# Kernel tuning notes

Hardware: AMD Instinct MI355X
Metric: run time of the kernel (lower is better)

The kernel has to match this reference:

```python
import jax, jax.numpy as jnp
import numpy as np

NUM_HEADS = 12
EMB = 768
D_KEY = 64
D_VALUE = 64
MASKED = True


def setup_inputs() -> dict:
    key = jax.random.key(0)
    k1, k2, k3, k4 = jax.random.split(key, 4)
    x = jax.random.normal(k1, (1, 4096, EMB), dtype=jnp.float32)
    q_proj = jax.random.normal(k2, (NUM_HEADS, EMB, D_KEY), dtype=jnp.float32)
    k_proj = jax.random.normal(k3, (NUM_HEADS, EMB, D_KEY), dtype=jnp.float32)
    v_proj = jax.random.normal(k4, (NUM_HEADS, EMB, D_VALUE), dtype=jnp.float32)
    return {"x": x, "q_proj": q_proj, "k_proj": k_proj, "v_proj": v_proj}


def reference(x, q_proj, k_proj, v_proj):
    # x: [B, S, E]; projections: [H, E, dk/dv]
    q = jnp.einsum("bse,hek->bhsk", x, q_proj)  # [B,H,S,dk]
    k = jnp.einsum("bse,hek->bhsk", x, k_proj)  # [B,H,S,dk]
    v = jnp.einsum("bse,hev->bhsv", x, v_proj)  # [B,H,S,dv]
    scale = jnp.sqrt(jnp.asarray(D_KEY, dtype=x.dtype))
    scores = jnp.einsum("bhsk,bhtk->bhst", q, k) / scale  # [B,H,S,S]
    if MASKED:
        S = x.shape[1]
        # causal mask: disallow attending to future positions (strict upper triangle)
        mask = jnp.triu(jnp.ones((S, S), dtype=bool), k=1)
        scores = jnp.where(mask, -jnp.inf, scores)
    attn = jax.nn.softmax(scores, axis=-1)
    out = jnp.einsum("bhst,bhtv->bhsv", attn, v)  # [B,H,S,dv]
    return out
```

## Files before the change

### kernel.cpp

```cpp
#include <hip/hip_runtime.h>
#include <hip/hip_bf16.h>

#define NH 12
#define SEQ 4096
#define E 768
#define DK 64

typedef float f32x4 __attribute__((ext_vector_type(4)));
typedef float f32x16 __attribute__((ext_vector_type(16)));
typedef __bf16 bf16x8 __attribute__((ext_vector_type(8)));
typedef __bf16 bf16x4 __attribute__((ext_vector_type(4)));
typedef unsigned u32x2 __attribute__((ext_vector_type(2)));
typedef unsigned u32x4 __attribute__((ext_vector_type(4)));

#define MFMA16(a, b, c) __builtin_amdgcn_mfma_f32_16x16x32_bf16((a), (b), (c), 0, 0, 0)
#define MFMA32(a, b, c) __builtin_amdgcn_mfma_f32_32x32x16_bf16((a), (b), (c), 0, 0, 0)

#define SCL 0.18033688011112042f
#define DEFER 10.8f

#define PART_SZ 4352
#define TPH 144

__device__ __forceinline__ void gload16(const void* g, void* l) {
    __builtin_amdgcn_global_load_lds(
        (const __attribute__((address_space(1))) void*)g,
        (__attribute__((address_space(3))) void*)l, 16, 0, 0);
}

__device__ __forceinline__ void block_sync() {
    __builtin_amdgcn_sched_barrier(0);
    __builtin_amdgcn_s_barrier();
    __builtin_amdgcn_sched_barrier(0);
}

__device__ __forceinline__ unsigned cvtpk(float lo, float hi) {
    unsigned r;
    asm("v_cvt_pk_bf16_f32 %0, %1, %2" : "=v"(r) : "v"(lo), "v"(hi));
    return r;
}
__device__ __forceinline__ u32x2 plswap(unsigned a, unsigned b) {
    return __builtin_amdgcn_permlane32_swap(a, b, false, false);
}
__device__ __forceinline__ float xhalf_max(float v) {
    u32x2 r = plswap(__float_as_uint(v), __float_as_uint(v));
    return fmaxf(__uint_as_float(r.x), __uint_as_float(r.y));
}
__device__ __forceinline__ float xhalf_add(float v) {
    u32x2 r = plswap(__float_as_uint(v), __float_as_uint(v));
    return __uint_as_float(r.x) + __uint_as_float(r.y);
}

__global__ __launch_bounds__(256) void xsplit_kernel(const float* __restrict__ x,
                                                     __bf16* __restrict__ xh,
                                                     __bf16* __restrict__ xl) {
    int i = blockIdx.x * blockDim.x + threadIdx.x;
    float4 v = ((const float4*)x)[i];
    bf16x4 h, l;
    float vv[4] = {v.x, v.y, v.z, v.w};
#pragma unroll
    for (int j = 0; j < 4; ++j) {
        __bf16 hh = (__bf16)vv[j];
        h[j] = hh;
        l[j] = (__bf16)(vv[j] - (float)hh);
    }
    ((bf16x4*)xh)[i] = h;
    ((bf16x4*)xl)[i] = l;
}

__global__ void wsplit_kernel(const float* __restrict__ qp,
                              const float* __restrict__ kp,
                              const float* __restrict__ vp,
                              __bf16* __restrict__ wtq_h, __bf16* __restrict__ wtq_l,
                              __bf16* __restrict__ wtk_h, __bf16* __restrict__ wtk_l,
                              __bf16* __restrict__ wtv_h) {
    int idx = blockIdx.x * blockDim.x + threadIdx.x;
    if (idx >= NH * E * DK) return;
    int h = idx / (E * DK);
    int rem = idx - h * E * DK;
    int k = rem / DK;
    int n = rem - k * DK;
    int o = h * DK * E + n * E + k;
    float q = qp[idx];
    __bf16 qh = (__bf16)q;
    wtq_h[o] = qh;
    wtq_l[o] = (__bf16)(q - (float)qh);
    float kk = kp[idx] * SCL;
    __bf16 kh = (__bf16)kk;
    wtk_h[o] = kh;
    wtk_l[o] = (__bf16)(kk - (float)kh);
    wtv_h[o] = (__bf16)vp[idx];
}

__global__ __launch_bounds__(256, 2) void proj_kernel(
    const __bf16* __restrict__ xh, const __bf16* __restrict__ xl,
    const __bf16* __restrict__ wq_h_g, const __bf16* __restrict__ wq_l_g,
    const __bf16* __restrict__ wk_h_g, const __bf16* __restrict__ wk_l_g,
    const __bf16* __restrict__ wv_g,
    __bf16* __restrict__ qh_o, __bf16* __restrict__ ql_o,
    __bf16* __restrict__ kh_o, __bf16* __restrict__ kl_o,
    __bf16* __restrict__ vt_o) {
    __shared__ char wlds[2][20480];

    const int wg = (blockIdx.x & 7) * 96 + (blockIdx.x >> 3);
    const int head = wg >> 6;
    const int rb = wg & 63;
    const int wave = threadIdx.x >> 6;
    const int lane = threadIdx.x & 63;
    const int lrow = lane & 15;
    const int lk8 = (lane >> 4) * 8;
    const int g4 = (lane >> 4) * 4;
    const int rowbase = rb * 64 + wave * 16;

    const char* bases[5] = {
        (const char*)(wq_h_g + head * DK * E), (const char*)(wq_l_g + head * DK * E),
        (const char*)(wk_h_g + head * DK * E), (const char*)(wk_l_g + head * DK * E),
        (const char*)(wv_g + head * DK * E)};
    const int srow = lane >> 2;
    const int scol = (lane & 3) * 16;

    auto STAGE = [&](int buf, int ks) {
#pragma unroll
        for (int r = 0; r < 5; ++r) {
            int q = wave * 5 + r;
            const char* src = bases[q >> 2] + (size_t)((q & 3) * 16 + srow) * (E * 2) + ks * 64 + scol;
            gload16(src, wlds[buf] + q * 1024 + lane * 16);
        }
    };

    f32x4 accq[4], acck[4], accv[4];
#pragma unroll
    for (int f = 0; f < 4; ++f) {
        accq[f] = (f32x4){0.f, 0.f, 0.f, 0.f};
        acck[f] = (f32x4){0.f, 0.f, 0.f, 0.f};
        accv[f] = (f32x4){0.f, 0.f, 0.f, 0.f};
    }

    bf16x8 ah, al, ahn, aln;
    auto LOADA = [&](int ks, bf16x8& h, bf16x8& l) {
        size_t xo = (size_t)(rowbase + lrow) * E + ks * 32 + lk8;
        h = *(const bf16x8*)(xh + xo);
        l = *(const bf16x8*)(xl + xo);
    };

    LOADA(0, ah, al);
    STAGE(0, 0);
    int buf = 0;
    for (int ks = 0; ks < 24; ++ks) {
        if (ks < 23) {
            LOADA(ks + 1, ahn, aln);
            STAGE(buf ^ 1, ks + 1);
            asm volatile("s_waitcnt vmcnt(7)" ::: "memory");
        } else {
            asm volatile("s_waitcnt vmcnt(0)" ::: "memory");
        }
        block_sync();
#pragma unroll
        for (int f = 0; f < 4; ++f) {
            int bo = (f * 16 + lrow) * 64 + lk8 * 2;
            bf16x8 bqh = *(const bf16x8*)(wlds[buf] + bo);
            bf16x8 bql = *(const bf16x8*)(wlds[buf] + 4096 + bo);
            bf16x8 bkh = *(const bf16x8*)(wlds[buf] + 8192 + bo);
            bf16x8 bkl = *(const bf16x8*)(wlds[buf] + 12288 + bo);
            bf16x8 bv  = *(const bf16x8*)(wlds[buf] + 16384 + bo);
            accq[f] = MFMA16(ah, bqh, accq[f]);
            accq[f] = MFMA16(ah, bql, accq[f]);
            accq[f] = MFMA16(al, bqh, accq[f]);
            acck[f] = MFMA16(ah, bkh, acck[f]);
            acck[f] = MFMA16(ah, bkl, acck[f]);
            acck[f] = MFMA16(al, bkh, acck[f]);
            accv[f] = MFMA16(bv, ah, accv[f]);
        }
        block_sync();
        if (ks < 23) {
            ah = ahn;
            al = aln;
        }
        buf ^= 1;
    }

    char* khb = (char*)kh_o + (size_t)head * SEQ * DK * 2;
    char* klb = (char*)kl_o + (size_t)head * SEQ * DK * 2;
    char* vb = (char*)vt_o + (size_t)head * DK * SEQ * 2;
#pragma unroll
    for (int f = 0; f < 4; ++f)
#pragma unroll
        for (int r = 0; r < 4; ++r) {
            int srow_o = rowbase + g4 + r;
            int d = f * 16 + lrow;
            size_t o = (size_t)head * SEQ * DK + (size_t)srow_o * DK + d;
            float qv = accq[f][r];
            __bf16 qhh = (__bf16)qv;
            qh_o[o] = qhh;
            ql_o[o] = (__bf16)(qv - (float)qhh);
            size_t ko = (size_t)(srow_o >> 6) * 8192 + ((srow_o >> 5) & 1) * 4096
                      + (size_t)f * 1024
                      + ((srow_o & 31) + 32 * ((lrow >> 3) & 1)) * 16 + (lrow & 7) * 2;
            float kv = acck[f][r];
            __bf16 khh = (__bf16)kv;
            *(__bf16*)(khb + ko) = khh;
            *(__bf16*)(klb + ko) = (__bf16)(kv - (float)khh);
            int vd = f * 16 + g4 + r;
            int vs = rowbase + lrow;
            size_t vo = (size_t)(vs >> 6) * 8192 + ((vd >> 5) & 1) * 4096
                      + ((vs >> 4) & 3) * 1024
                      + ((vd & 31) + 32 * ((vs >> 3) & 1)) * 16 + (vs & 7) * 2;
            *(__bf16*)(vb + vo) = (__bf16)accv[f][r];
        }
}

__global__ __launch_bounds__(256, 2) void attn_part_kernel(
    const __bf16* __restrict__ qh, const __bf16* __restrict__ ql,
    const __bf16* __restrict__ kh, const __bf16* __restrict__ kl,
    const __bf16* __restrict__ vt,
    char* __restrict__ part) {
    __shared__ char kvlds[2][24576];

    const int blk = (blockIdx.x & 7) * 216 + (blockIdx.x >> 3);
    const int head = blk / TPH;
    const int t = TPH - 1 - (blk - head * TPH);
    int g = 0, base = 0;
    for (int gg = 1; gg < 32; ++gg) {
        int qq = gg >> 2, rr = gg & 3;
        int b = 2 * qq * (qq + 1) + rr * (qq + 1);
        if (t >= b) { g = gg; base = b; }
    }
    const int s = t - base;
    const int nsp = (g + 4) >> 2;
    const int ktot = 2 * g + 2;
    const int lo = (s * ktot) / nsp;
    const int hi = ((s + 1) * ktot) / nsp;

    const int wave = threadIdx.x >> 6;
    const int lane = threadIdx.x & 63;
    const int lq = lane & 31;
    const int lh = lane >> 5;
    const int rowbase = (4 * g + wave) * 32;

    const size_t hoff = (size_t)head * SEQ * DK;

    bf16x8 qBh[4], qBl[4];
    {
        const __bf16* qph = qh + hoff + (size_t)(rowbase + lq) * DK + lh * 8;
        const __bf16* qpl = ql + hoff + (size_t)(rowbase + lq) * DK + lh * 8;
#pragma unroll
        for (int ds = 0; ds < 4; ++ds) {
            qBh[ds] = *(const bf16x8*)(qph + ds * 16);
            qBl[ds] = *(const bf16x8*)(qpl + ds * 16);
        }
    }
    asm volatile("s_waitcnt vmcnt(0)" ::: "memory");

    const char* kh_b = (const char*)(kh + hoff);
    const char* kl_b = (const char*)(kl + hoff);
    const char* vt_b = (const char*)(vt + (size_t)head * DK * SEQ);

    auto STAGE = [&](int buf, int tile) {
#pragma unroll
        for (int r = 0; r < 6; ++r) {
            int q = wave * 6 + r;
            const char* src;
            if (q < 8)       src = kh_b + (size_t)tile * 8192 + q * 1024;
            else if (q < 16) src = kl_b + (size_t)tile * 8192 + (q - 8) * 1024;
            else             src = vt_b + (size_t)tile * 8192 + (q - 16) * 1024;
            gload16(src + lane * 16, kvlds[buf] + q * 1024);
        }
    };

    f32x16 O0 = (f32x16)0.0f, O1 = (f32x16)0.0f;
    float m = -3.0e38f, lsum = 0.f;

    STAGE(0, lo);
    int buf = 0;
    for (int tt = lo; tt < hi; ++tt) {
        if (tt + 1 < hi) {
            STAGE(buf ^ 1, tt + 1);
            asm volatile("s_waitcnt vmcnt(6)" ::: "memory");
        } else {
            asm volatile("s_waitcnt vmcnt(0)" ::: "memory");
        }
        block_sync();

        const int kb = tt * 64;
        if (kb <= rowbase + 31) {
            const char* Khl = kvlds[buf];
            const char* Kll = kvlds[buf] + 8192;
            const char* Vtl = kvlds[buf] + 16384;

            f32x16 s0 = (f32x16)0.0f, s1 = (f32x16)0.0f;
#pragma unroll
            for (int ds = 0; ds < 4; ++ds) {
                bf16x8 ah0 = *(const bf16x8*)(Khl + ds * 1024 + lane * 16);
                bf16x8 al0 = *(const bf16x8*)(Kll + ds * 1024 + lane * 16);
                bf16x8 ah1 = *(const bf16x8*)(Khl + 4096 + ds * 1024 + lane * 16);
                bf16x8 al1 = *(const bf16x8*)(Kll + 4096 + ds * 1024 + lane * 16);
                s0 = MFMA32(ah0, qBh[ds], s0);
                s1 = MFMA32(ah1, qBh[ds], s1);
                s0 = MFMA32(al0, qBh[ds], s0);
                s1 = MFMA32(al1, qBh[ds], s1);
                s0 = MFMA32(ah0, qBl[ds], s0);
                s1 = MFMA32(ah1, qBl[ds], s1);
            }

            if (kb + 63 > rowbase) {
                int qa = rowbase + lq;
#pragma unroll
                for (int r = 0; r < 16; ++r) {
                    int kp = kb + ((r & 3) + 8 * (r >> 2) + 4 * lh);
                    if (kp > qa) s0[r] = -1.0e30f;
                    if (kp + 32 > qa) s1[r] = -1.0e30f;
                }
            }

            float x0 = fmaxf(s0[0], s0[1]), x1 = fmaxf(s0[2], s0[3]);
            float x2 = fmaxf(s0[4], s0[5]), x3 = fmaxf(s0[6], s0[7]);
#pragma unroll
            for (int r = 8; r < 16; r += 4) {
                x0 = fmaxf(x0, fmaxf(s0[r], s0[r + 1]));
                x1 = fmaxf(x1, fmaxf(s0[r + 2], s0[r + 3]));
            }
#pragma unroll
            for (int r = 0; r < 16; r += 4) {
                x2 = fmaxf(x2, fmaxf(s1[r], s1[r + 1]));
                x3 = fmaxf(x3, fmaxf(s1[r + 2], s1[r + 3]));
            }
            float mx = xhalf_max(fmaxf(fmaxf(x0, x1), fmaxf(x2, x3)));

            if (!__all(mx - m <= DEFER)) {
                float mn = fmaxf(m, mx);
                float al = exp2f(m - mn);
                m = mn;
                lsum *= al;
#pragma unroll
                for (int r = 0; r < 16; ++r) {
                    float a = __shfl(al, (r & 3) + 8 * (r >> 2) + 4 * lh);
                    O0[r] *= a;
                    O1[r] *= a;
                }
            }

            s0 = s0 - m;
            s1 = s1 - m;
#pragma unroll
            for (int r = 0; r < 16; ++r) {
                s0[r] = exp2f(s0[r]);
                s1[r] = exp2f(s1[r]);
            }
            {
                f32x16 sv = s0 + s1;
                float p0 = 0.f, p1 = 0.f;
#pragma unroll
                for (int r = 0; r < 16; r += 4) {
                    p0 += sv[r] + sv[r + 1];
                    p1 += sv[r + 2] + sv[r + 3];
                }
                lsum += p0 + p1;
            }

            unsigned W0 = cvtpk(s0[0], s0[1]), W1 = cvtpk(s0[2], s0[3]);
            unsigned W2 = cvtpk(s0[4], s0[5]), W3 = cvtpk(s0[6], s0[7]);
            unsigned W4 = cvtpk(s0[8], s0[9]), W5 = cvtpk(s0[10], s0[11]);
            unsigned W6 = cvtpk(s0[12], s0[13]), W7 = cvtpk(s0[14], s0[15]);
            u32x2 rA = plswap(W0, W2), rB = plswap(W1, W3);
            u32x2 rC = plswap(W4, W6), rD = plswap(W5, W7);
            bf16x8 p00 = __builtin_bit_cast(bf16x8, (u32x4){rA.x, rB.x, rA.y, rB.y});
            bf16x8 p01 = __builtin_bit_cast(bf16x8, (u32x4){rC.x, rD.x, rC.y, rD.y});
            W0 = cvtpk(s1[0], s1[1]); W1 = cvtpk(s1[2], s1[3]);
            W2 = cvtpk(s1[4], s1[5]); W3 = cvtpk(s1[6], s1[7]);
            W4 = cvtpk(s1[8], s1[9]); W5 = cvtpk(s1[10], s1[11]);
            W6 = cvtpk(s1[12], s1[13]); W7 = cvtpk(s1[14], s1[15]);
            rA = plswap(W0, W2); rB = plswap(W1, W3);
            rC = plswap(W4, W6); rD = plswap(W5, W7);
            bf16x8 p10 = __builtin_bit_cast(bf16x8, (u32x4){rA.x, rB.x, rA.y, rB.y});
            bf16x8 p11 = __builtin_bit_cast(bf16x8, (u32x4){rC.x, rD.x, rC.y, rD.y});

            {
                bf16x8 v00 = *(const bf16x8*)(Vtl + 0 + lane * 16);
                bf16x8 v01 = *(const bf16x8*)(Vtl + 1024 + lane * 16);
                bf16x8 v10 = *(const bf16x8*)(Vtl + 2048 + lane * 16);
                bf16x8 v11 = *(const bf16x8*)(Vtl + 3072 + lane * 16);
                O0 = MFMA32(p00, v00, O0);
                O0 = MFMA32(p01, v01, O0);
                O0 = MFMA32(p10, v10, O0);
                O0 = MFMA32(p11, v11, O0);
                bf16x8 w00 = *(const bf16x8*)(Vtl + 4096 + lane * 16);
                bf16x8 w01 = *(const bf16x8*)(Vtl + 5120 + lane * 16);
                bf16x8 w10 = *(const bf16x8*)(Vtl + 6144 + lane * 16);
                bf16x8 w11 = *(const bf16x8*)(Vtl + 7168 + lane * 16);
                O1 = MFMA32(p00, w00, O1);
                O1 = MFMA32(p01, w01, O1);
                O1 = MFMA32(p10, w10, O1);
                O1 = MFMA32(p11, w11, O1);
            }
        }

        block_sync();
        buf ^= 1;
    }

    char* pb = part + ((size_t)(head * TPH + t) * 4 + wave) * PART_SZ;
    unsigned* ph = (unsigned*)pb;
#pragma unroll
    for (int r = 0; r < 16; r += 2) {
        ph[(r >> 1) * 64 + lane] = cvtpk(O0[r], O0[r + 1]);
        ph[512 + (r >> 1) * 64 + lane] = cvtpk(O1[r], O1[r + 1]);
    }
    float lf = xhalf_add(lsum);
    float* pm = (float*)(pb + 4096);
    if (lane < 32) {
        pm[lq] = m;
        pm[32 + lq] = lf;
    }
}

__global__ __launch_bounds__(256) void attn_comb_kernel(
    const char* __restrict__ part, float* __restrict__ out) {
    const int W = blockIdx.x;
    const int head = W >> 7, w = W & 127;
    const int g = w >> 2;
    const int qq = g >> 2, rr = g & 3;
    const int base_g = 2 * qq * (qq + 1) + rr * (qq + 1);
    const int nsp = (g + 4) >> 2;

    const int tid = threadIdx.x;
    const int row = tid >> 3;
    const int d0 = (tid & 7) * 8;
    const int lane0 = (d0 & 31) + 32 * ((row >> 2) & 1);
    const int r = (row & 3) + 4 * (row >> 3);
    const int word = (r >> 1) * 64;
    const int hi16 = r & 1;
    const char* p0 = part + ((size_t)(head * TPH + base_g) * 4 + (w & 3)) * PART_SZ;

    float mstar = -3.0e38f;
    for (int s = 0; s < nsp; ++s) {
        const float* pm = (const float*)(p0 + (size_t)s * 4 * PART_SZ + 4096);
        mstar = fmaxf(mstar, pm[row]);
    }

    float acc[8] = {0.f, 0.f, 0.f, 0.f, 0.f, 0.f, 0.f, 0.f};
    float lt = 0.f;
    for (int s = 0; s < nsp; ++s) {
        const char* ps = p0 + (size_t)s * 4 * PART_SZ;
        const float* pm = (const float*)(ps + 4096);
        float wgt = exp2f(pm[row] - mstar);
        lt += wgt * pm[32 + row];
        const unsigned* pw = (const unsigned*)(ps + (d0 >> 5) * 2048);
        u32x4 a = *(const u32x4*)(pw + word + lane0);
        u32x4 b = *(const u32x4*)(pw + word + lane0 + 4);
#pragma unroll
        for (int j = 0; j < 8; ++j) {
            unsigned u = (j < 4) ? a[j] : b[j - 4];
            unsigned bits = hi16 ? (u & 0xffff0000u) : (u << 16);
            acc[j] += wgt * __uint_as_float(bits);
        }
    }
    float inv = 1.0f / lt;
    size_t o = (size_t)head * SEQ * DK + (size_t)(w * 32 + row) * DK + d0;
#pragma unroll
    for (int j = 0; j < 8; ++j) out[o + j] = acc[j] * inv;
}

extern "C" void kernel_launch(void* const* d_in, const int* in_sizes, int n_in,
                              void* d_out, int out_size, void* d_ws, size_t ws_size,
                              hipStream_t stream) {
    const float* x = (const float*)d_in[0];
    const float* qp = (const float*)d_in[1];
    const float* kp = (const float*)d_in[2];
    const float* vp = (const float*)d_in[3];
    float* out = (float*)d_out;

    const size_t WT_SZ = (size_t)NH * DK * E * 2;
    const size_t QKV_SZ = (size_t)NH * SEQ * DK * 2;
    const size_t X_SZ = (size_t)SEQ * E * 2;
    char* ws = (char*)d_ws;
    __bf16* wtq_h = (__bf16*)(ws + 0 * WT_SZ);
    __bf16* wtq_l = (__bf16*)(ws + 1 * WT_SZ);
    __bf16* wtk_h = (__bf16*)(ws + 2 * WT_SZ);
    __bf16* wtk_l = (__bf16*)(ws + 3 * WT_SZ);
    __bf16* wtv_h = (__bf16*)(ws + 4 * WT_SZ);
    char* px = ws + 5 * WT_SZ;
    __bf16* xh = (__bf16*)(px + 0 * X_SZ);
    __bf16* xl = (__bf16*)(px + 1 * X_SZ);
    char* p2 = px + 2 * X_SZ;
    __bf16* qh = (__bf16*)(p2 + 0 * QKV_SZ);
    __bf16* ql = (__bf16*)(p2 + 1 * QKV_SZ);
    __bf16* kh = (__bf16*)(p2 + 2 * QKV_SZ);
    __bf16* kl = (__bf16*)(p2 + 3 * QKV_SZ);
    __bf16* vt = (__bf16*)(p2 + 4 * QKV_SZ);
    char* part = p2 + 5 * QKV_SZ;

    hipLaunchKernelGGL(xsplit_kernel, dim3(SEQ * E / 4 / 256), dim3(256), 0, stream,
                       x, xh, xl);
    hipLaunchKernelGGL(wsplit_kernel, dim3((NH * E * DK + 255) / 256), dim3(256), 0, stream,
                       qp, kp, vp, wtq_h, wtq_l, wtk_h, wtk_l, wtv_h);
    hipLaunchKernelGGL(proj_kernel, dim3(768), dim3(256), 0, stream,
                       xh, xl, wtq_h, wtq_l, wtk_h, wtk_l, wtv_h, qh, ql, kh, kl, vt);
    hipLaunchKernelGGL(attn_part_kernel, dim3(1728), dim3(256), 0, stream,
                       qh, ql, kh, kl, vt, part);
    hipLaunchKernelGGL(attn_comb_kernel, dim3(1536), dim3(256), 0, stream,
                       part, out);
}
```

Baseline: 165.9 us.

## Use 8-wave attention blocks sharing KV tiles, and tile-transpose weight split

```diff
diff --git a/kernel.cpp b/kernel.cpp
--- a/kernel.cpp
+++ b/kernel.cpp
@@ -20,7 +20,7 @@
 #define DEFER 10.8f
 
 #define PART_SZ 4352
-#define TPH 144
+#define TPH 72
 
 __device__ __forceinline__ void gload16(const void* g, void* l) {
     __builtin_amdgcn_global_load_lds(
@@ -68,28 +68,48 @@
     ((bf16x4*)xl)[i] = l;
 }
 
-__global__ void wsplit_kernel(const float* __restrict__ qp,
-                              const float* __restrict__ kp,
-                              const float* __restrict__ vp,
-                              __bf16* __restrict__ wtq_h, __bf16* __restrict__ wtq_l,
-                              __bf16* __restrict__ wtk_h, __bf16* __restrict__ wtk_l,
-                              __bf16* __restrict__ wtv_h) {
-    int idx = blockIdx.x * blockDim.x + threadIdx.x;
-    if (idx >= NH * E * DK) return;
-    int h = idx / (E * DK);
-    int rem = idx - h * E * DK;
-    int k = rem / DK;
-    int n = rem - k * DK;
-    int o = h * DK * E + n * E + k;
-    float q = qp[idx];
-    __bf16 qh = (__bf16)q;
-    wtq_h[o] = qh;
-    wtq_l[o] = (__bf16)(q - (float)qh);
-    float kk = kp[idx] * SCL;
-    __bf16 kh = (__bf16)kk;
-    wtk_h[o] = kh;
-    wtk_l[o] = (__bf16)(kk - (float)kh);
-    wtv_h[o] = (__bf16)vp[idx];
+__global__ __launch_bounds__(256) void wsplit_kernel(
+    const float* __restrict__ qp, const float* __restrict__ kp,
+    const float* __restrict__ vp,
+    __bf16* __restrict__ wtq_h, __bf16* __restrict__ wtq_l,
+    __bf16* __restrict__ wtk_h, __bf16* __restrict__ wtk_l,
+    __bf16* __restrict__ wtv_h) {
+    __shared__ float tl[64][65];
+    const int h = blockIdx.x / 12;
+    const int kt = blockIdx.x % 12;
+    const int c = threadIdx.x & 63;
+    const int r4 = threadIdx.x >> 6;
+
+#pragma unroll
+    for (int mat = 0; mat < 3; ++mat) {
+        const float* src = ((mat == 0) ? qp : (mat == 1) ? kp : vp)
+                         + (size_t)h * E * DK + (size_t)kt * 64 * DK;
+        __syncthreads();
+#pragma unroll
+        for (int i = 0; i < 16; ++i) {
+            int row = i * 4 + r4;
+            tl[row][c] = src[row * DK + c];
+        }
+        __syncthreads();
+#pragma unroll
+        for (int i = 0; i < 16; ++i) {
+            int n = i * 4 + r4;
+            float v = tl[c][n];
+            size_t o = (size_t)h * DK * E + (size_t)n * E + kt * 64 + c;
+            if (mat == 0) {
+                __bf16 hh = (__bf16)v;
+                wtq_h[o] = hh;
+                wtq_l[o] = (__bf16)(v - (float)hh);
+            } else if (mat == 1) {
+                float kk = v * SCL;
+                __bf16 hh = (__bf16)kk;
+                wtk_h[o] = hh;
+                wtk_l[o] = (__bf16)(kk - (float)hh);
+            } else {
+                wtv_h[o] = (__bf16)v;
+            }
+        }
+    }
 }
 
 __global__ __launch_bounds__(256, 2) void proj_kernel(
@@ -209,25 +229,24 @@
         }
 }
 
-__global__ __launch_bounds__(256, 2) void attn_part_kernel(
+__global__ __launch_bounds__(512, 2) void attn_part_kernel(
     const __bf16* __restrict__ qh, const __bf16* __restrict__ ql,
     const __bf16* __restrict__ kh, const __bf16* __restrict__ kl,
     const __bf16* __restrict__ vt,
     char* __restrict__ part) {
     __shared__ char kvlds[2][24576];
 
-    const int blk = (blockIdx.x & 7) * 216 + (blockIdx.x >> 3);
+    const int blk = (blockIdx.x & 7) * 108 + (blockIdx.x >> 3);
     const int head = blk / TPH;
     const int t = TPH - 1 - (blk - head * TPH);
-    int g = 0, base = 0;
-    for (int gg = 1; gg < 32; ++gg) {
-        int qq = gg >> 2, rr = gg & 3;
-        int b = 2 * qq * (qq + 1) + rr * (qq + 1);
-        if (t >= b) { g = gg; base = b; }
-    }
+    int G = 0;
+#pragma unroll
+    for (int gg = 1; gg < 16; ++gg)
+        if (t >= (((gg + 1) * (gg + 1)) >> 2)) G = gg;
+    const int base = ((G + 1) * (G + 1)) >> 2;
     const int s = t - base;
-    const int nsp = (g + 4) >> 2;
-    const int ktot = 2 * g + 2;
+    const int nsp = (G + 2) >> 1;
+    const int ktot = 4 * (G + 1);
     const int lo = (s * ktot) / nsp;
     const int hi = ((s + 1) * ktot) / nsp;
 
@@ -235,7 +254,7 @@
     const int lane = threadIdx.x & 63;
     const int lq = lane & 31;
     const int lh = lane >> 5;
-    const int rowbase = (4 * g + wave) * 32;
+    const int rowbase = (8 * G + wave) * 32;
 
     const size_t hoff = (size_t)head * SEQ * DK;
 
@@ -257,8 +276,8 @@
 
     auto STAGE = [&](int buf, int tile) {
 #pragma unroll
-        for (int r = 0; r < 6; ++r) {
-            int q = wave * 6 + r;
+        for (int r = 0; r < 3; ++r) {
+            int q = wave * 3 + r;
             const char* src;
             if (q < 8)       src = kh_b + (size_t)tile * 8192 + q * 1024;
             else if (q < 16) src = kl_b + (size_t)tile * 8192 + (q - 8) * 1024;
@@ -275,7 +294,7 @@
     for (int tt = lo; tt < hi; ++tt) {
         if (tt + 1 < hi) {
             STAGE(buf ^ 1, tt + 1);
-            asm volatile("s_waitcnt vmcnt(6)" ::: "memory");
+            asm volatile("s_waitcnt vmcnt(3)" ::: "memory");
         } else {
             asm volatile("s_waitcnt vmcnt(0)" ::: "memory");
         }
@@ -398,7 +417,7 @@
         buf ^= 1;
     }
 
-    char* pb = part + ((size_t)(head * TPH + t) * 4 + wave) * PART_SZ;
+    char* pb = part + ((size_t)(head * TPH + t) * 8 + wave) * PART_SZ;
     unsigned* ph = (unsigned*)pb;
 #pragma unroll
     for (int r = 0; r < 16; r += 2) {
@@ -417,10 +436,9 @@
     const char* __restrict__ part, float* __restrict__ out) {
     const int W = blockIdx.x;
     const int head = W >> 7, w = W & 127;
-    const int g = w >> 2;
-    const int qq = g >> 2, rr = g & 3;
-    const int base_g = 2 * qq * (qq + 1) + rr * (qq + 1);
-    const int nsp = (g + 4) >> 2;
+    const int G = w >> 3;
+    const int base = ((G + 1) * (G + 1)) >> 2;
+    const int nsp = (G + 2) >> 1;
 
     const int tid = threadIdx.x;
     const int row = tid >> 3;
@@ -429,18 +447,18 @@
     const int r = (row & 3) + 4 * (row >> 3);
     const int word = (r >> 1) * 64;
     const int hi16 = r & 1;
-    const char* p0 = part + ((size_t)(head * TPH + base_g) * 4 + (w & 3)) * PART_SZ;
+    const char* p0 = part + ((size_t)(head * TPH + base) * 8 + (w & 7)) * PART_SZ;
 
     float mstar = -3.0e38f;
     for (int s = 0; s < nsp; ++s) {
-        const float* pm = (const float*)(p0 + (size_t)s * 4 * PART_SZ + 4096);
+        const float* pm = (const float*)(p0 + (size_t)s * 8 * PART_SZ + 4096);
         mstar = fmaxf(mstar, pm[row]);
     }
 
     float acc[8] = {0.f, 0.f, 0.f, 0.f, 0.f, 0.f, 0.f, 0.f};
     float lt = 0.f;
     for (int s = 0; s < nsp; ++s) {
-        const char* ps = p0 + (size_t)s * 4 * PART_SZ;
+        const char* ps = p0 + (size_t)s * 8 * PART_SZ;
         const float* pm = (const float*)(ps + 4096);
         float wgt = exp2f(pm[row] - mstar);
         lt += wgt * pm[32 + row];
@@ -491,11 +509,11 @@
 
     hipLaunchKernelGGL(xsplit_kernel, dim3(SEQ * E / 4 / 256), dim3(256), 0, stream,
                        x, xh, xl);
-    hipLaunchKernelGGL(wsplit_kernel, dim3((NH * E * DK + 255) / 256), dim3(256), 0, stream,
+    hipLaunchKernelGGL(wsplit_kernel, dim3(144), dim3(256), 0, stream,
                        qp, kp, vp, wtq_h, wtq_l, wtk_h, wtk_l, wtv_h);
     hipLaunchKernelGGL(proj_kernel, dim3(768), dim3(256), 0, stream,
                        xh, xl, wtq_h, wtq_l, wtk_h, wtk_l, wtv_h, qh, ql, kh, kl, vt);
-    hipLaunchKernelGGL(attn_part_kernel, dim3(1728), dim3(256), 0, stream,
+    hipLaunchKernelGGL(attn_part_kernel, dim3(864), dim3(512), 0, stream,
                        qh, ql, kh, kl, vt, part);
     hipLaunchKernelGGL(attn_comb_kernel, dim3(1536), dim3(256), 0, stream,
                        part, out);
```

After: 172.5 us. 4.0% more time.
